# Kernel tuning notes

Measured on AMD Instinct MI355X. Metric: run time of the kernel, lower is better.

Reference implementation:

```python
import jax, jax.numpy as jnp
import numpy as np
from jax.experimental.jet import jet

ORDER = 3  # Taylor order from init_kwargs
D, C, H = 4096, 4096, 8192


def setup_inputs() -> dict:
    key = jax.random.key(0)
    k = jax.random.split(key, 6)
    sc1 = 1.0 / np.sqrt(D + C)
    sc2 = 1.0 / np.sqrt(H)
    return {
        "h": jax.random.normal(k[0], (D,), jnp.float32),
        "r": jnp.zeros((), jnp.float32),  # ignored residual slot of h_r tuple
        "t": jax.random.uniform(k[1], (), jnp.float32),
        "c": jax.random.normal(k[2], (C,), jnp.float32),
        "W1": jax.random.normal(k[3], (D + C, H), jnp.float32) * sc1,
        "b1": jnp.zeros((H,), jnp.float32),
        "W2": jax.random.normal(k[4], (H, D), jnp.float32) * sc2,
        "b2": jnp.zeros((D,), jnp.float32),
    }


def reference(h, r, t, c, W1, b1, W2, b2):
    # dynamics f(h, t, c): 2-layer tanh MLP on concat(h, c)
    def f(_h, _t, _c):
        x = jnp.concatenate((_h, _c))
        return jnp.tanh(x @ W1 + b1) @ W2 + b2

    h_shape = h.shape

    def g(h_t):
        # expand flattened state+time through dynamics
        _h, _t = jnp.reshape(h_t[:-1], h_shape), h_t[-1]
        dh = jnp.ravel(f(_h, _t, c))
        return jnp.concatenate((dh, jnp.array([1.0], dtype=dh.dtype)))

    h_t = jnp.concatenate((jnp.ravel(h), jnp.reshape(t, (1,))))
    # recursive Taylor-mode jet expansion
    (y0, [*yns]) = jet(g, (h_t,), ((jnp.ones_like(h_t),),))
    for _ in range(ORDER - 1):
        (y0, [*yns]) = jet(g, (h_t,), ((y0, *yns),))
    dydt = jnp.reshape(y0[:-1], h_shape)
    drdt = jnp.reshape(yns[-2][:-1], h_shape)
    return (dydt, jnp.mean(drdt ** 2))
```

## Files before the change

### kernel.cpp

```cpp
#include <hip/hip_runtime.h>

#define DD 4096
#define CC 4096
#define HH 8192


__global__ __launch_bounds__(256) void ew_concat(const float* __restrict__ h,
                                                 const float* __restrict__ c,
                                                 float* __restrict__ x0) {
    int i = blockIdx.x * 256 + threadIdx.x;
    x0[i] = (i < DD) ? h[i] : c[i - DD];
}

__global__ __launch_bounds__(256) void ew_tanh(const float* __restrict__ a0,
                                               const float* __restrict__ b1,
                                               float* __restrict__ s0,
                                               float* __restrict__ t0) {
    int i = blockIdx.x * 256 + threadIdx.x;
    float s = tanhf(a0[i] + b1[i]);
    s0[i] = s;
    t0[i] = 1.0f - s * s;
}

__global__ __launch_bounds__(256) void ew_addb_out(const float* __restrict__ Fr,
                                                   const float* __restrict__ b2,
                                                   float* __restrict__ Ff,
                                                   float* __restrict__ dout) {
    int i = blockIdx.x * 256 + threadIdx.x;
    float f = Fr[i] + b2[i];
    Ff[i] = f;
    dout[i] = f;
}

__global__ __launch_bounds__(256) void ew_mul(const float* __restrict__ t0,
                                              const float* __restrict__ a1,
                                              float* __restrict__ p1) {
    int i = blockIdx.x * 256 + threadIdx.x;
    p1[i] = t0[i] * a1[i];
}

__global__ __launch_bounds__(256) void ew_s2(const float* __restrict__ t0,
                                             const float* __restrict__ s0,
                                             const float* __restrict__ a1,
                                             const float* __restrict__ a2,
                                             float* __restrict__ s2) {
    int i = blockIdx.x * 256 + threadIdx.x;
    float a1v = a1[i];
    s2[i] = t0[i] * (a2[i] - s0[i] * a1v * a1v);
}


__global__ __launch_bounds__(256) void gemv_acc(const float* __restrict__ W,
                                                const float* __restrict__ x,
                                                float* __restrict__ out,
                                                int N, int KS) {
    const int ncol = blockIdx.x * 1024 + threadIdx.x * 4;
    const int k0 = blockIdx.y * KS;
    const float* Wp = W + (size_t)k0 * (size_t)N + ncol;
    const float* xp = x + k0;

    float ax = 0.f, ay = 0.f, az = 0.f, aw = 0.f;
#pragma unroll 4
    for (int k = 0; k < KS; ++k) {
        float xv = xp[k];
        float4 w = *reinterpret_cast<const float4*>(Wp + (size_t)k * (size_t)N);
        ax = fmaf(xv, w.x, ax);
        ay = fmaf(xv, w.y, ay);
        az = fmaf(xv, w.z, az);
        aw = fmaf(xv, w.w, aw);
    }
    float* op = out + ncol;
    atomicAdd(op + 0, ax);
    atomicAdd(op + 1, ay);
    atomicAdd(op + 2, az);
    atomicAdd(op + 3, aw);
}


__global__ __launch_bounds__(256) void reduce_meansq(const float* __restrict__ C2v,
                                                     float* __restrict__ dout) {
    float s = 0.f;
    for (int i = threadIdx.x; i < DD; i += 256) {
        float v = C2v[i];
        s = fmaf(v, v, s);
    }
    for (int off = 32; off; off >>= 1) s += __shfl_down(s, off);
    __shared__ float ls[4];
    int wid = threadIdx.x >> 6;
    if ((threadIdx.x & 63) == 0) ls[wid] = s;
    __syncthreads();
    if (threadIdx.x == 0) {
        float tot = ls[0] + ls[1] + ls[2] + ls[3];
        dout[DD] = tot / (float)DD;
    }
}


extern "C" void kernel_launch(void* const* d_in, const int* in_sizes, int n_in,
                              void* d_out, int out_size, void* d_ws, size_t ws_size,
                              hipStream_t stream) {
    const float* h  = (const float*)d_in[0];
    const float* c  = (const float*)d_in[3];
    const float* W1 = (const float*)d_in[4];
    const float* b1 = (const float*)d_in[5];
    const float* W2 = (const float*)d_in[6];
    const float* b2 = (const float*)d_in[7];

    float* out = (float*)d_out;
    float* ws = (float*)d_ws;

    float* a0 = ws + 0;
    float* Fr = ws + 8192;
    float* a1 = ws + 12288;
    float* v  = ws + 20480;
    float* a2 = ws + 24576;
    float* C2 = ws + 32768;
    float* x0 = ws + 36864;
    float* s0 = ws + 45056;
    float* t0 = ws + 53248;
    float* Ff = ws + 61440;
    float* p1 = ws + 65536;
    float* s2 = ws + 73728;

    hipMemsetAsync(ws, 0, 36864 * sizeof(float), stream);

    ew_concat<<<32, 256, 0, stream>>>(h, c, x0);
    gemv_acc<<<dim3(8, 64), 256, 0, stream>>>(W1, x0, a0, HH, 128);
    ew_tanh<<<32, 256, 0, stream>>>(a0, b1, s0, t0);
    gemv_acc<<<dim3(4, 128), 256, 0, stream>>>(W2, s0, Fr, DD, 64);
    ew_addb_out<<<16, 256, 0, stream>>>(Fr, b2, Ff, out);
    gemv_acc<<<dim3(8, 64), 256, 0, stream>>>(W1, Ff, a1, HH, 64);
    ew_mul<<<32, 256, 0, stream>>>(t0, a1, p1);
    gemv_acc<<<dim3(4, 128), 256, 0, stream>>>(W2, p1, v, DD, 64);
    gemv_acc<<<dim3(8, 64), 256, 0, stream>>>(W1, v, a2, HH, 64);
    ew_s2<<<32, 256, 0, stream>>>(t0, s0, a1, a2, s2);
    gemv_acc<<<dim3(4, 128), 256, 0, stream>>>(W2, s2, C2, DD, 64);
    reduce_meansq<<<1, 256, 0, stream>>>(C2, out);
}
```

Before: 240.1 us.

## Replace atomic split-K GEMVs with partial buffers reduced in the next fused stage

Each split-K GEMV now writes its per-slice partial sums to a workspace buffer instead of using atomicAdd. The next GEMV stage reduces those partials for its own K slice and applies the elementwise step (concat, tanh, bias, multiply, s2) before staging the input vector in shared memory. This removes the memset, the atomics and the separate elementwise launches. In exchange, every column block re-reads the partials and the workspace grows to several megabytes per stage. Some split sizes and vector widths also change.

```diff
diff --git a/kernel.cpp b/kernel.cpp
--- a/kernel.cpp
+++ b/kernel.cpp
@@ -1,81 +1,107 @@
 #include <hip/hip_runtime.h>
 
 #define DD 4096
-#define CC 4096
 #define HH 8192
 
+enum Stage { S_X0 = 0, S_TANH, S_BIASOUT, S_PMUL, S_COPY, S_S2 };
 
-__global__ __launch_bounds__(256) void ew_concat(const float* __restrict__ h,
-                                                 const float* __restrict__ c,
-                                                 float* __restrict__ x0) {
-    int i = blockIdx.x * 256 + threadIdx.x;
-    x0[i] = (i < DD) ? h[i] : c[i - DD];
+template <int STAGE, int KS, int SPREV, int KPREV, int NTOT, int CPT>
+__global__ __launch_bounds__(256) void gemv_stage(
+    const float* __restrict__ W,
+    const float* __restrict__ Pprev,
+    float* __restrict__ Pout,
+    const float* __restrict__ h, const float* __restrict__ c,
+    const float* __restrict__ b1, const float* __restrict__ b2,
+    float* __restrict__ s0g, float* __restrict__ t0g, float* __restrict__ a1g,
+    float* __restrict__ outv)
+{
+    constexpr int GROUPS = 256 / KS;
+    __shared__ float xs[KS];
+    __shared__ float part[GROUPS][KS];
+
+    const int tid = threadIdx.x;
+    const int k0 = blockIdx.y * KS;
+
+    if constexpr (STAGE == S_X0) {
+        if (tid < KS) {
+            int k = k0 + tid;
+            xs[tid] = (k < DD) ? h[k] : c[k - DD];
+        }
+    } else {
+        const int g = tid / KS;
+        const int j = tid % KS;
+        float acc = 0.f;
+        for (int s = g; s < SPREV; s += GROUPS)
+            acc += Pprev[(size_t)s * KPREV + k0 + j];
+        part[g][j] = acc;
+        __syncthreads();
+        if (tid < KS) {
+            const int k = k0 + tid;
+            float tot = 0.f;
+#pragma unroll
+            for (int g2 = 0; g2 < GROUPS; ++g2) tot += part[g2][tid];
+            float xv;
+            if constexpr (STAGE == S_TANH) {
+                float s = tanhf(tot + b1[k]);
+                float t = 1.f - s * s;
+                xv = s;
+                if (blockIdx.x == 0) { s0g[k] = s; t0g[k] = t; }
+            } else if constexpr (STAGE == S_BIASOUT) {
+                xv = tot + b2[k];
+                if (blockIdx.x == 0) outv[k] = xv;
+            } else if constexpr (STAGE == S_PMUL) {
+                xv = t0g[k] * tot;
+                if (blockIdx.x == 0) a1g[k] = tot;
+            } else if constexpr (STAGE == S_COPY) {
+                xv = tot;
+            } else {
+                float a1v = a1g[k];
+                xv = t0g[k] * (tot - s0g[k] * a1v * a1v);
+            }
+            xs[tid] = xv;
+        }
+    }
+    __syncthreads();
+
+    if constexpr (CPT == 4) {
+        const int ncol = blockIdx.x * 1024 + tid * 4;
+        const float* Wp = W + (size_t)k0 * NTOT + ncol;
+        float ax = 0.f, ay = 0.f, az = 0.f, aw = 0.f;
+#pragma unroll 8
+        for (int k = 0; k < KS; ++k) {
+            float xv = xs[k];
+            float4 w = *reinterpret_cast<const float4*>(Wp + (size_t)k * NTOT);
+            ax = fmaf(xv, w.x, ax);
+            ay = fmaf(xv, w.y, ay);
+            az = fmaf(xv, w.z, az);
+            aw = fmaf(xv, w.w, aw);
+        }
+        *reinterpret_cast<float4*>(Pout + (size_t)blockIdx.y * NTOT + ncol) =
+            make_float4(ax, ay, az, aw);
+    } else {
+        const int ncol = blockIdx.x * 512 + tid * 2;
+        const float* Wp = W + (size_t)k0 * NTOT + ncol;
+        float ax = 0.f, ay = 0.f;
+#pragma unroll 8
+        for (int k = 0; k < KS; ++k) {
+            float xv = xs[k];
+            float2 w = *reinterpret_cast<const float2*>(Wp + (size_t)k * NTOT);
+            ax = fmaf(xv, w.x, ax);
+            ay = fmaf(xv, w.y, ay);
+        }
+        *reinterpret_cast<float2*>(Pout + (size_t)blockIdx.y * NTOT + ncol) =
+            make_float2(ax, ay);
+    }
 }
 
-__global__ __launch_bounds__(256) void ew_tanh(const float* __restrict__ a0,
-                                               const float* __restrict__ b1,
-                                               float* __restrict__ s0,
-                                               float* __restrict__ t0) {
-    int i = blockIdx.x * 256 + threadIdx.x;
-    float s = tanhf(a0[i] + b1[i]);
-    s0[i] = s;
-    t0[i] = 1.0f - s * s;
+__global__ __launch_bounds__(256) void reduce_C2(const float* __restrict__ P6,
+                                                 float* __restrict__ C2) {
+    int n = blockIdx.x * 256 + threadIdx.x;
+    float acc = 0.f;
+#pragma unroll 8
+    for (int s = 0; s < 128; ++s) acc += P6[(size_t)s * DD + n];
+    C2[n] = acc;
 }
-
-__global__ __launch_bounds__(256) void ew_addb_out(const float* __restrict__ Fr,
-                                                   const float* __restrict__ b2,
-                                                   float* __restrict__ Ff,
-                                                   float* __restrict__ dout) {
-    int i = blockIdx.x * 256 + threadIdx.x;
-    float f = Fr[i] + b2[i];
-    Ff[i] = f;
-    dout[i] = f;
-}
-
-__global__ __launch_bounds__(256) void ew_mul(const float* __restrict__ t0,
-                                              const float* __restrict__ a1,
-                                              float* __restrict__ p1) {
-    int i = blockIdx.x * 256 + threadIdx.x;
-    p1[i] = t0[i] * a1[i];
-}
-
-__global__ __launch_bounds__(256) void ew_s2(const float* __restrict__ t0,
-                                             const float* __restrict__ s0,
-                                             const float* __restrict__ a1,
-                                             const float* __restrict__ a2,
-                                             float* __restrict__ s2) {
-    int i = blockIdx.x * 256 + threadIdx.x;
-    float a1v = a1[i];
-    s2[i] = t0[i] * (a2[i] - s0[i] * a1v * a1v);
-}
-
-
-__global__ __launch_bounds__(256) void gemv_acc(const float* __restrict__ W,
-                                                const float* __restrict__ x,
-                                                float* __restrict__ out,
-                                                int N, int KS) {
-    const int ncol = blockIdx.x * 1024 + threadIdx.x * 4;
-    const int k0 = blockIdx.y * KS;
-    const float* Wp = W + (size_t)k0 * (size_t)N + ncol;
-    const float* xp = x + k0;
-
-    float ax = 0.f, ay = 0.f, az = 0.f, aw = 0.f;
-#pragma unroll 4
-    for (int k = 0; k < KS; ++k) {
-        float xv = xp[k];
-        float4 w = *reinterpret_cast<const float4*>(Wp + (size_t)k * (size_t)N);
-        ax = fmaf(xv, w.x, ax);
-        ay = fmaf(xv, w.y, ay);
-        az = fmaf(xv, w.z, az);
-        aw = fmaf(xv, w.w, aw);
-    }
-    float* op = out + ncol;
-    atomicAdd(op + 0, ax);
-    atomicAdd(op + 1, ay);
-    atomicAdd(op + 2, az);
-    atomicAdd(op + 3, aw);
-}
-
 
 __global__ __launch_bounds__(256) void reduce_meansq(const float* __restrict__ C2v,
                                                      float* __restrict__ dout) {
@@ -90,11 +116,9 @@
     if ((threadIdx.x & 63) == 0) ls[wid] = s;
     __syncthreads();
     if (threadIdx.x == 0) {
-        float tot = ls[0] + ls[1] + ls[2] + ls[3];
-        dout[DD] = tot / (float)DD;
+        dout[DD] = (ls[0] + ls[1] + ls[2] + ls[3]) / (float)DD;
     }
 }
-
 
 extern "C" void kernel_launch(void* const* d_in, const int* in_sizes, int n_in,
                               void* d_out, int out_size, void* d_ws, size_t ws_size,
@@ -105,35 +129,32 @@
     const float* b1 = (const float*)d_in[5];
     const float* W2 = (const float*)d_in[6];
     const float* b2 = (const float*)d_in[7];
-
     float* out = (float*)d_out;
     float* ws = (float*)d_ws;
 
-    float* a0 = ws + 0;
-    float* Fr = ws + 8192;
-    float* a1 = ws + 12288;
-    float* v  = ws + 20480;
-    float* a2 = ws + 24576;
-    float* C2 = ws + 32768;
-    float* x0 = ws + 36864;
-    float* s0 = ws + 45056;
-    float* t0 = ws + 53248;
-    float* Ff = ws + 61440;
-    float* p1 = ws + 65536;
-    float* s2 = ws + 73728;
+    float* P1 = ws;
+    float* P2 = P1 + 1048576;
+    float* P3 = P2 + 524288;
+    float* P4 = P3 + 1048576;
+    float* P5 = P4 + 524288;
+    float* P6 = P5 + 1048576;
+    float* s0 = P6 + 524288;
+    float* t0 = s0 + 8192;
+    float* a1 = t0 + 8192;
+    float* C2 = a1 + 8192;
 
-    hipMemsetAsync(ws, 0, 36864 * sizeof(float), stream);
-
-    ew_concat<<<32, 256, 0, stream>>>(h, c, x0);
-    gemv_acc<<<dim3(8, 64), 256, 0, stream>>>(W1, x0, a0, HH, 128);
-    ew_tanh<<<32, 256, 0, stream>>>(a0, b1, s0, t0);
-    gemv_acc<<<dim3(4, 128), 256, 0, stream>>>(W2, s0, Fr, DD, 64);
-    ew_addb_out<<<16, 256, 0, stream>>>(Fr, b2, Ff, out);
-    gemv_acc<<<dim3(8, 64), 256, 0, stream>>>(W1, Ff, a1, HH, 64);
-    ew_mul<<<32, 256, 0, stream>>>(t0, a1, p1);
-    gemv_acc<<<dim3(4, 128), 256, 0, stream>>>(W2, p1, v, DD, 64);
-    gemv_acc<<<dim3(8, 64), 256, 0, stream>>>(W1, v, a2, HH, 64);
-    ew_s2<<<32, 256, 0, stream>>>(t0, s0, a1, a2, s2);
-    gemv_acc<<<dim3(4, 128), 256, 0, stream>>>(W2, s2, C2, DD, 64);
+    gemv_stage<S_X0, 64, 1, 1, HH, 4><<<dim3(8, 128), 256, 0, stream>>>(
+        W1, nullptr, P1, h, c, b1, b2, s0, t0, a1, out);
+    gemv_stage<S_TANH, 64, 128, HH, DD, 2><<<dim3(8, 128), 256, 0, stream>>>(
+        W2, P1, P2, h, c, b1, b2, s0, t0, a1, out);
+    gemv_stage<S_BIASOUT, 32, 128, DD, HH, 4><<<dim3(8, 128), 256, 0, stream>>>(
+        W1, P2, P3, h, c, b1, b2, s0, t0, a1, out);
+    gemv_stage<S_PMUL, 64, 128, HH, DD, 2><<<dim3(8, 128), 256, 0, stream>>>(
+        W2, P3, P4, h, c, b1, b2, s0, t0, a1, out);
+    gemv_stage<S_COPY, 32, 128, DD, HH, 4><<<dim3(8, 128), 256, 0, stream>>>(
+        W1, P4, P5, h, c, b1, b2, s0, t0, a1, out);
+    gemv_stage<S_S2, 64, 128, HH, DD, 2><<<dim3(8, 128), 256, 0, stream>>>(
+        W2, P5, P6, h, c, b1, b2, s0, t0, a1, out);
+    reduce_C2<<<16, 256, 0, stream>>>(P6, C2);
     reduce_meansq<<<1, 256, 0, stream>>>(C2, out);
 }
```

Result: faster. 214.6 us (-10.6%).
